# Kernel tuning notes

Measured on AMD Instinct MI355X. Metric: run time of the kernel, lower is better.

The kernel has to match this reference:

```python
import jax, jax.numpy as jnp
import numpy as np

RADIUS = 0.2
NPOINT = 1024
NSAMPLE = 32


def _square_distance(src, dst):
    # src [B,S,C], dst [B,N,C] -> [B,S,N]
    d = -2.0 * jnp.einsum('bsc,bnc->bsn', src, dst)
    d = d + jnp.sum(src * src, -1)[:, :, None]
    d = d + jnp.sum(dst * dst, -1)[:, None, :]
    return d


def _index_points(points, idx):
    # points [B,N,C], idx [B,...] int -> [B,...,C]
    B = points.shape[0]
    flat = idx.reshape(B, -1)
    out = jnp.take_along_axis(points, flat[:, :, None], axis=1)
    return out.reshape(idx.shape + (points.shape[-1],))


def _query_ball_point(radius, nsample, xyz, new_xyz):
    # xyz [B,N,C], new_xyz [B,S,C] -> idx [B,S,nsample]
    B, N, _ = xyz.shape
    sqd = _square_distance(new_xyz, xyz)            # [B,S,N]
    base = jnp.arange(N, dtype=jnp.int32)[None, None, :]
    idx = jnp.where(sqd > radius * radius, N, base)  # out-of-ball -> sentinel N
    idx = jnp.sort(idx, axis=-1)[:, :, :nsample]     # nearest-index nsample in ball
    first = idx[:, :, :1]
    idx = jnp.where(idx == N, first, idx)            # pad with first valid index
    return idx


def setup_inputs() -> dict:
    key = jax.random.key(0)
    ks = jax.random.split(key, 4)
    B, N, D = 8, 8192, 64
    xyz = jax.random.normal(ks[0], (B, 2, N), dtype=jnp.float32)
    points = jax.random.normal(ks[1], (B, D, N), dtype=jnp.float32)
    C_in = D + 2
    W1 = jax.random.normal(ks[2], (128, C_in), dtype=jnp.float32) * (1.0 / np.sqrt(C_in))
    b1 = jnp.zeros((128,), dtype=jnp.float32)
    W2 = jax.random.normal(ks[3], (256, 128), dtype=jnp.float32) * (1.0 / np.sqrt(128))
    b2 = jnp.zeros((256,), dtype=jnp.float32)
    return {"xyz": xyz, "points": points, "W1": W1, "b1": b1, "W2": W2, "b2": b2}


def reference(xyz, points, W1, b1, W2, b2):
    # xyz [B,2,N], points [B,D,N]
    xyz_t = jnp.transpose(xyz, (0, 2, 1))        # [B,N,2]
    pts_t = jnp.transpose(points, (0, 2, 1))     # [B,N,D]
    B, N, C = xyz_t.shape
    S = NPOINT
    # fps_idx = arange(npoint) in the source (deterministic sampling)
    new_xyz = xyz_t[:, :S, :]                    # [B,S,2]
    idx = _query_ball_point(RADIUS, NSAMPLE, xyz_t, new_xyz)   # [B,S,K]
    grouped_xyz = _index_points(xyz_t, idx)                    # [B,S,K,2]
    grouped_xyz_norm = grouped_xyz - new_xyz[:, :, None, :]
    grouped_pts = _index_points(pts_t, idx)                    # [B,S,K,D]
    feat = jnp.concatenate([grouped_xyz_norm, grouped_pts], axis=-1)  # [B,S,K,2+D]
    # permute(0,3,2,1) -> [B, C, K, S]; conv kernel (1,1) == pointwise linear on C
    h = jnp.transpose(feat, (0, 3, 2, 1))                      # [B,C,K,S]
    h = jax.nn.silu(jnp.einsum('bcks,oc->boks', h, W1) + b1[None, :, None, None])
    h = jax.nn.silu(jnp.einsum('bcks,oc->boks', h, W2) + b2[None, :, None, None])
    return h.mean(axis=2)                                      # [B, 256, S]
```

## Files before the change

### kernel.cpp

```cpp
#include <hip/hip_runtime.h>
#include <math.h>

#define BB 8
#define NN 8192
#define SS 1024
#define NS 32
#define DD 64
#define C1 128
#define C2 256
#define R2 0.04f
#define CPB 8

using bf16x8 = __attribute__((ext_vector_type(8))) short;
using f32x4  = __attribute__((ext_vector_type(4))) float;

__device__ __forceinline__ float silu_f(float x) {
    return x / (1.0f + __expf(-x));
}
__device__ __forceinline__ unsigned int f2bf(float f) {
    unsigned int u = __float_as_uint(f);
    u += 0x7fffu + ((u >> 16) & 1u);
    return u >> 16;
}
__device__ __forceinline__ float bfl(unsigned int u) { return __uint_as_float(u << 16); }
__device__ __forceinline__ float bfh(unsigned int u) { return __uint_as_float(u & 0xffff0000u); }

__global__ __launch_bounds__(256) void qbp_kernel(const float* __restrict__ xyz,
                                                  int* __restrict__ idx_ws) {
    int gwave = (blockIdx.x * blockDim.x + threadIdx.x) >> 6;
    int lane  = threadIdx.x & 63;
    int b = gwave >> 10;
    int s = gwave & (SS - 1);
    const float* x = xyz + (size_t)b * 2 * NN;
    const float* y = x + NN;
    float cx = x[s], cy = y[s];
    float cs = __fadd_rn(__fmul_rn(cx, cx), __fmul_rn(cy, cy));
    int* ob = idx_ws + ((size_t)(b * SS + s)) * NS;

    int written = 0;
    int first = -1;
    for (int base = 0; base < NN && written < NS; base += 128) {
        int jA = base + lane, jB = base + 64 + lane;
        float pxA = x[jA], pyA = y[jA];
        float pxB = x[jB], pyB = y[jB];
        float ppA = __fadd_rn(__fmul_rn(pxA, pxA), __fmul_rn(pyA, pyA));
        float eA  = __fadd_rn(__fmul_rn(cx, pxA), __fmul_rn(cy, pyA));
        float dA  = __fadd_rn(__fadd_rn(__fmul_rn(-2.0f, eA), cs), ppA);
        float ppB = __fadd_rn(__fmul_rn(pxB, pxB), __fmul_rn(pyB, pyB));
        float eB  = __fadd_rn(__fmul_rn(cx, pxB), __fmul_rn(cy, pyB));
        float dB  = __fadd_rn(__fadd_rn(__fmul_rn(-2.0f, eB), cs), ppB);
        bool inA = !(dA > R2);
        bool inB = !(dB > R2);
        unsigned long long mA = __ballot(inA);
        unsigned long long mB = __ballot(inB);
        if (first < 0) {
            if (mA)      first = base + (__ffsll(mA) - 1);
            else if (mB) first = base + 64 + (__ffsll(mB) - 1);
        }
        unsigned long long below = (1ull << lane) - 1ull;
        int posA = __popcll(mA & below);
        if (inA && written + posA < NS) ob[written + posA] = jA;
        int wA = written + __popcll(mA);
        int posB = __popcll(mB & below);
        if (inB && wA + posB < NS) ob[wA + posB] = jB;
        written = wA + __popcll(mB);
        if (written > NS) written = NS;
    }
    if (lane >= written && lane < NS) ob[lane] = first;
}

__global__ __launch_bounds__(256) void pack_kernel(const float* __restrict__ W1,
                                                   const float* __restrict__ W2,
                                                   unsigned short* __restrict__ W1p,
                                                   unsigned short* __restrict__ W2p) {
    int bid = blockIdx.x;
    if (bid < 16) {
        int tid = bid * 256 + threadIdx.x;
        int l = tid & 63, frag = tid >> 6;
        int kb = frag >> 4, nt = frag & 15;
        int o  = nt * 16 + (l & 15);
        int c0 = kb * 32 + ((l >> 4) << 3);
        const float* src = W2 + (size_t)o * C1 + c0;
        unsigned int up[4];
        #pragma unroll
        for (int q = 0; q < 4; ++q)
            up[q] = f2bf(src[2 * q]) | (f2bf(src[2 * q + 1]) << 16);
        *(uint4*)(W2p + ((size_t)tid << 3)) = make_uint4(up[0], up[1], up[2], up[3]);
    } else {
        int tid = (bid - 16) * 256 + threadIdx.x;
        int l = tid & 63, frag = tid >> 6;
        int kb = frag >> 3, nt = frag & 7;
        int o  = nt * 16 + (l & 15);
        int c0 = kb * 32 + ((l >> 4) << 3);
        const float* src = W1 + (size_t)o * 66 + 2 + c0;
        unsigned int up[4];
        #pragma unroll
        for (int q = 0; q < 4; ++q)
            up[q] = f2bf(src[2 * q]) | (f2bf(src[2 * q + 1]) << 16);
        *(uint4*)(W1p + ((size_t)tid << 3)) = make_uint4(up[0], up[1], up[2], up[3]);
    }
}

__global__ __launch_bounds__(256) void p1g_kernel(const float* __restrict__ points,
                                                  const unsigned short* __restrict__ W1p,
                                                  const float* __restrict__ b1,
                                                  unsigned short* __restrict__ P1) {
    __shared__ __align__(16) char lds[34816];
    const int t = threadIdx.x;
    const int w = t >> 6, l = t & 63;
    const int bidx = blockIdx.x;
    const int b  = bidx >> 6;
    const int j0 = (bidx & 63) << 7;

    bf16x8 bfr[8][2];
    #pragma unroll
    for (int nt = 0; nt < 8; ++nt)
        #pragma unroll
        for (int kb = 0; kb < 2; ++kb)
            bfr[nt][kb] = *(const bf16x8*)(W1p + (((size_t)((kb * 8 + nt) * 64 + l)) << 3));
    float b1v[8];
    #pragma unroll
    for (int nt = 0; nt < 8; ++nt) b1v[nt] = b1[nt * 16 + (l & 15)];

    {
        const float* pb = points + (size_t)b * DD * NN + j0;
        int jj0 = (t & 31) * 4;
        #pragma unroll
        for (int i = 0; i < 4; ++i) {
            int c = 2 * ((t >> 5) + i * 8);
            float4 q0 = *(const float4*)(pb + (size_t)c * NN + jj0);
            float4 q1 = *(const float4*)(pb + (size_t)(c + 1) * NN + jj0);
            float a0[4] = {q0.x, q0.y, q0.z, q0.w};
            float a1[4] = {q1.x, q1.y, q1.z, q1.w};
            #pragma unroll
            for (int d = 0; d < 4; ++d) {
                int jj = jj0 + d;
                unsigned int u = f2bf(a0[d]) | (f2bf(a1[d]) << 16);
                unsigned int addr = ((unsigned)(jj * 128 + c * 2))
                                    ^ ((unsigned)((((jj & 7) ^ ((jj >> 2) & 7)) << 4)));
                *(unsigned int*)(lds + addr) = u;
            }
        }
    }
    __syncthreads();

    bf16x8 afr[2][2];
    #pragma unroll
    for (int mt = 0; mt < 2; ++mt)
        #pragma unroll
        for (int kb = 0; kb < 2; ++kb) {
            int jg = w * 32 + mt * 16 + (l & 15);
            unsigned int addr = ((unsigned)(jg * 128 + kb * 64 + ((l >> 4) << 4)))
                                ^ ((unsigned)((((jg & 7) ^ ((jg >> 2) & 7)) << 4)));
            afr[mt][kb] = *(const bf16x8*)(lds + addr);
        }
    __syncthreads();

    f32x4 acc[2][8];
    #pragma unroll
    for (int mt = 0; mt < 2; ++mt)
        #pragma unroll
        for (int nt = 0; nt < 8; ++nt) {
            f32x4 z4 = {0.0f, 0.0f, 0.0f, 0.0f};
            acc[mt][nt] = z4;
        }
    #pragma unroll
    for (int kb = 0; kb < 2; ++kb)
        #pragma unroll
        for (int mt = 0; mt < 2; ++mt)
            #pragma unroll
            for (int nt = 0; nt < 8; ++nt)
                acc[mt][nt] = __builtin_amdgcn_mfma_f32_16x16x32_bf16(
                    afr[mt][kb], bfr[nt][kb], acc[mt][nt], 0, 0, 0);

    #pragma unroll
    for (int mt = 0; mt < 2; ++mt)
        #pragma unroll
        for (int nt = 0; nt < 8; ++nt) {
            int row0 = w * 32 + mt * 16 + ((l >> 4) << 2);
            int col  = nt * 16 + (l & 15);
            #pragma unroll
            for (int r = 0; r < 4; ++r) {
                float v = acc[mt][nt][r] + b1v[nt];
                *(unsigned short*)(lds + (size_t)(row0 + r) * 272 + col * 2) =
                    (unsigned short)f2bf(v);
            }
        }
    __syncthreads();

    {
        int row = t >> 1, half = t & 1;
        const char* src = lds + (size_t)row * 272 + half * 128;
        unsigned short* dst = P1 + ((size_t)(b * NN + j0 + row)) * C1 + half * 64;
        #pragma unroll
        for (int i = 0; i < 8; ++i)
            *(uint4*)(dst + i * 8) = *(const uint4*)(src + i * 16);
    }
}

__global__ __launch_bounds__(256) void fused2_kernel(const float* __restrict__ xyz,
                                                     const float* __restrict__ W1,
                                                     const float* __restrict__ b2,
                                                     const unsigned short* __restrict__ P1,
                                                     const int* __restrict__ idx_ws,
                                                     const unsigned short* __restrict__ W2p,
                                                     float* __restrict__ tmp) {
    __shared__ __align__(16) unsigned short H1s[NS * C1];
    __shared__ int   idxs[CPB][NS];
    __shared__ float dxs[CPB][NS], dys[CPB][NS];
    __shared__ float w1xy[2][C1];

    const int t = threadIdx.x;
    const int w = t >> 6, l = t & 63;
    const int gc0 = blockIdx.x * CPB;

    if (t < C1) { w1xy[0][t] = W1[(size_t)t * 66 + 0]; w1xy[1][t] = W1[(size_t)t * 66 + 1]; }
    {
        int ci = t >> 5, kk = t & 31;
        int gc = gc0 + ci;
        int b = gc >> 10, s = gc & (SS - 1);
        const float* x = xyz + (size_t)b * 2 * NN;
        const float* y = x + NN;
        int j = idx_ws[(size_t)gc * NS + kk];
        idxs[ci][kk] = j;
        dxs[ci][kk] = x[j] - x[s];
        dys[ci][kk] = y[j] - y[s];
    }

    bf16x8 bfr[4][4];
    #pragma unroll
    for (int kb = 0; kb < 4; ++kb)
        #pragma unroll
        for (int ntl = 0; ntl < 4; ++ntl) {
            int nt = w * 4 + ntl;
            bfr[ntl][kb] = *(const bf16x8*)(W2p + ((size_t)((kb * 16 + nt) * 64 + l) << 3));
        }
    float b2v[4];
    #pragma unroll
    for (int ntl = 0; ntl < 4; ++ntl) b2v[ntl] = b2[w * 64 + ntl * 16 + (l & 15)];

    __syncthreads();

    const int k = t >> 3, cb = t & 7;
    for (int ci = 0; ci < CPB; ++ci) {
        int gc = gc0 + ci;
        int b = gc >> 10;
        {
            int j = idxs[ci][k];
            float dx = dxs[ci][k], dy = dys[ci][k];
            const uint4* pr = (const uint4*)(P1 + ((size_t)b * NN + j) * C1 + cb * 16);
            uint4 q0 = pr[0], q1 = pr[1];
            float hv[16];
            hv[0]  = bfl(q0.x); hv[1]  = bfh(q0.x);
            hv[2]  = bfl(q0.y); hv[3]  = bfh(q0.y);
            hv[4]  = bfl(q0.z); hv[5]  = bfh(q0.z);
            hv[6]  = bfl(q0.w); hv[7]  = bfh(q0.w);
            hv[8]  = bfl(q1.x); hv[9]  = bfh(q1.x);
            hv[10] = bfl(q1.y); hv[11] = bfh(q1.y);
            hv[12] = bfl(q1.z); hv[13] = bfh(q1.z);
            hv[14] = bfl(q1.w); hv[15] = bfh(q1.w);
            #pragma unroll
            for (int i = 0; i < 16; ++i) {
                int c = cb * 16 + i;
                float v = hv[i] + w1xy[0][c] * dx + w1xy[1][c] * dy;
                hv[i] = silu_f(v);
            }
            unsigned int up[8];
            #pragma unroll
            for (int q = 0; q < 8; ++q)
                up[q] = f2bf(hv[2 * q]) | (f2bf(hv[2 * q + 1]) << 16);
            unsigned int swz = (unsigned)((k & 7) << 4);
            unsigned int a0 = ((unsigned)(k * 256 + cb * 32)) ^ swz;
            unsigned int a1 = ((unsigned)(k * 256 + cb * 32 + 16)) ^ swz;
            *(uint4*)((char*)H1s + a0) = make_uint4(up[0], up[1], up[2], up[3]);
            *(uint4*)((char*)H1s + a1) = make_uint4(up[4], up[5], up[6], up[7]);
        }
        __syncthreads();
        bf16x8 afr[2][4];
        #pragma unroll
        for (int mt = 0; mt < 2; ++mt)
            #pragma unroll
            for (int kb = 0; kb < 4; ++kb) {
                int m = mt * 16 + (l & 15);
                unsigned int addr = ((unsigned)(m * 256 + kb * 64 + ((l >> 4) << 4)))
                                    ^ ((unsigned)((m & 7) << 4));
                afr[mt][kb] = *(const bf16x8*)((char*)H1s + addr);
            }
        f32x4 acc[2][4];
        #pragma unroll
        for (int mt = 0; mt < 2; ++mt)
            #pragma unroll
            for (int ntl = 0; ntl < 4; ++ntl) {
                f32x4 z4 = {0.0f, 0.0f, 0.0f, 0.0f};
                acc[mt][ntl] = z4;
            }
        #pragma unroll
        for (int kb = 0; kb < 4; ++kb)
            #pragma unroll
            for (int mt = 0; mt < 2; ++mt)
                #pragma unroll
                for (int ntl = 0; ntl < 4; ++ntl)
                    acc[mt][ntl] = __builtin_amdgcn_mfma_f32_16x16x32_bf16(
                        afr[mt][kb], bfr[ntl][kb], acc[mt][ntl], 0, 0, 0);
        float po[4];
        #pragma unroll
        for (int ntl = 0; ntl < 4; ++ntl) {
            float sum = 0.0f;
            #pragma unroll
            for (int mt = 0; mt < 2; ++mt)
                #pragma unroll
                for (int r = 0; r < 4; ++r)
                    sum += silu_f(acc[mt][ntl][r] + b2v[ntl]);
            sum += __shfl_xor(sum, 16);
            sum += __shfl_xor(sum, 32);
            po[ntl] = sum * (1.0f / 32.0f);
        }
        if (l < 16) {
            #pragma unroll
            for (int ntl = 0; ntl < 4; ++ntl)
                tmp[(size_t)gc * C2 + w * 64 + ntl * 16 + l] = po[ntl];
        }
        __syncthreads();
    }
}

__global__ __launch_bounds__(256) void transpose_kernel(const float* __restrict__ tmp,
                                                        float* __restrict__ out) {
    __shared__ float tile[32][33];
    int bid = blockIdx.x;
    int b  = bid >> 8;
    int r  = bid & 255;
    int s0 = (r >> 3) << 5;
    int o0 = (r & 7) << 5;
    int t = threadIdx.x;
    int c = t & 31, rr = t >> 5;
    const float* tb = tmp + (size_t)b * SS * C2;
    #pragma unroll
    for (int i = 0; i < 4; ++i) {
        int row = rr + i * 8;
        tile[row][c] = tb[(size_t)(s0 + row) * C2 + o0 + c];
    }
    __syncthreads();
    float* ob = out + (size_t)b * C2 * SS;
    #pragma unroll
    for (int i = 0; i < 4; ++i) {
        int row = rr + i * 8;
        ob[(size_t)(o0 + row) * SS + s0 + c] = tile[c][row];
    }
}

extern "C" void kernel_launch(void* const* d_in, const int* in_sizes, int n_in,
                              void* d_out, int out_size, void* d_ws, size_t ws_size,
                              hipStream_t stream) {
    const float* xyz    = (const float*)d_in[0];
    const float* points = (const float*)d_in[1];
    const float* W1     = (const float*)d_in[2];
    const float* b1     = (const float*)d_in[3];
    const float* W2     = (const float*)d_in[4];
    const float* b2     = (const float*)d_in[5];
    float* out = (float*)d_out;

    const size_t OFF_W1P = 65536;
    const size_t OFF_IDX = OFF_W1P + 16384;
    const size_t OFF_P1  = OFF_IDX + (size_t)BB * SS * NS * sizeof(int);
    const size_t OFF_TMP = OFF_P1 + (size_t)BB * NN * C1 * sizeof(unsigned short);

    unsigned short* W2p = (unsigned short*)d_ws;
    unsigned short* W1p = (unsigned short*)((char*)d_ws + OFF_W1P);
    int*            idx = (int*)((char*)d_ws + OFF_IDX);
    unsigned short* P1  = (unsigned short*)((char*)d_ws + OFF_P1);
    float*          tmp = (float*)((char*)d_ws + OFF_TMP);

    qbp_kernel   <<<BB * SS / 4,     256, 0, stream>>>(xyz, idx);
    pack_kernel  <<<20,              256, 0, stream>>>(W1, W2, W1p, W2p);
    p1g_kernel   <<<BB * (NN / 128), 256, 0, stream>>>(points, W1p, b1, P1);
    fused2_kernel<<<BB * SS / CPB,   256, 0, stream>>>(xyz, W1, b2, P1, idx, W2p, tmp);
    transpose_kernel<<<BB * (SS / 32) * (C2 / 32), 256, 0, stream>>>(tmp, out);
}
```

Baseline: 187.7 us.

## Double-buffer H1 tiles, prefetch qbp loads, fast SiLU, halve centroids per block

The fused MLP kernel now double-buffers the H1 shared tile. The next centroid's gather and layer-1 SiLU overlap the current centroid's MFMA and reduction, with one barrier per iteration instead of two. The ball-query kernel software-prefetches the next chunk of coordinates. SiLU uses raw v_exp/v_rcp instructions, and centroids per block drop from 8 to 4, giving more blocks. The trade-offs are more LDS and registers per block and slightly less accurate exp and reciprocal.

```diff
diff --git a/kernel.cpp b/kernel.cpp
--- a/kernel.cpp
+++ b/kernel.cpp
@@ -9,13 +9,19 @@
 #define C1 128
 #define C2 256
 #define R2 0.04f
-#define CPB 8
+#define CPB 4
 
 using bf16x8 = __attribute__((ext_vector_type(8))) short;
 using f32x4  = __attribute__((ext_vector_type(4))) float;
 
+__device__ __forceinline__ float rcp_f(float v) {
+    float r; asm("v_rcp_f32 %0, %1" : "=v"(r) : "v"(v)); return r;
+}
+__device__ __forceinline__ float exp2_f(float v) {
+    float r; asm("v_exp_f32 %0, %1" : "=v"(r) : "v"(v)); return r;
+}
 __device__ __forceinline__ float silu_f(float x) {
-    return x / (1.0f + __expf(-x));
+    return x * rcp_f(1.0f + exp2_f(x * -1.44269504088896f));
 }
 __device__ __forceinline__ unsigned int f2bf(float f) {
     unsigned int u = __float_as_uint(f);
@@ -37,12 +43,17 @@
     float cs = __fadd_rn(__fmul_rn(cx, cx), __fmul_rn(cy, cy));
     int* ob = idx_ws + ((size_t)(b * SS + s)) * NS;
 
+    float pxA = x[lane],      pyA = y[lane];
+    float pxB = x[64 + lane], pyB = y[64 + lane];
+
     int written = 0;
     int first = -1;
     for (int base = 0; base < NN && written < NS; base += 128) {
-        int jA = base + lane, jB = base + 64 + lane;
-        float pxA = x[jA], pyA = y[jA];
-        float pxB = x[jB], pyB = y[jB];
+        int jA2 = base + 128 + lane;      if (jA2 >= NN) jA2 = NN - 1;
+        int jB2 = base + 192 + lane;      if (jB2 >= NN) jB2 = NN - 1;
+        float nxA = x[jA2], nyA = y[jA2];
+        float nxB = x[jB2], nyB = y[jB2];
+
         float ppA = __fadd_rn(__fmul_rn(pxA, pxA), __fmul_rn(pyA, pyA));
         float eA  = __fadd_rn(__fmul_rn(cx, pxA), __fmul_rn(cy, pyA));
         float dA  = __fadd_rn(__fadd_rn(__fmul_rn(-2.0f, eA), cs), ppA);
@@ -59,12 +70,14 @@
         }
         unsigned long long below = (1ull << lane) - 1ull;
         int posA = __popcll(mA & below);
-        if (inA && written + posA < NS) ob[written + posA] = jA;
+        if (inA && written + posA < NS) ob[written + posA] = base + lane;
         int wA = written + __popcll(mA);
         int posB = __popcll(mB & below);
-        if (inB && wA + posB < NS) ob[wA + posB] = jB;
+        if (inB && wA + posB < NS) ob[wA + posB] = base + 64 + lane;
         written = wA + __popcll(mB);
         if (written > NS) written = NS;
+
+        pxA = nxA; pyA = nyA; pxB = nxB; pyB = nyB;
     }
     if (lane >= written && lane < NS) ob[lane] = first;
 }
@@ -205,20 +218,24 @@
                                                      const int* __restrict__ idx_ws,
                                                      const unsigned short* __restrict__ W2p,
                                                      float* __restrict__ tmp) {
-    __shared__ __align__(16) unsigned short H1s[NS * C1];
+    __shared__ __align__(16) unsigned short H1s[2][NS * C1];
     __shared__ int   idxs[CPB][NS];
     __shared__ float dxs[CPB][NS], dys[CPB][NS];
-    __shared__ float w1xy[2][C1];
+    __shared__ float w1xy[C1][2];
 
     const int t = threadIdx.x;
     const int w = t >> 6, l = t & 63;
     const int gc0 = blockIdx.x * CPB;
-
-    if (t < C1) { w1xy[0][t] = W1[(size_t)t * 66 + 0]; w1xy[1][t] = W1[(size_t)t * 66 + 1]; }
-    {
+    const int b   = gc0 >> 10;
+
+    if (t < C1) {
+        w1xy[t][0] = W1[(size_t)t * 66 + 0];
+        w1xy[t][1] = W1[(size_t)t * 66 + 1];
+    }
+    if (t < CPB * NS) {
         int ci = t >> 5, kk = t & 31;
         int gc = gc0 + ci;
-        int b = gc >> 10, s = gc & (SS - 1);
+        int s = gc & (SS - 1);
         const float* x = xyz + (size_t)b * 2 * NN;
         const float* y = x + NN;
         int j = idx_ws[(size_t)gc * NS + kk];
@@ -242,14 +259,83 @@
     __syncthreads();
 
     const int k = t >> 3, cb = t & 7;
-    for (int ci = 0; ci < CPB; ++ci) {
-        int gc = gc0 + ci;
-        int b = gc >> 10;
-        {
-            int j = idxs[ci][k];
-            float dx = dxs[ci][k], dy = dys[ci][k];
-            const uint4* pr = (const uint4*)(P1 + ((size_t)b * NN + j) * C1 + cb * 16);
-            uint4 q0 = pr[0], q1 = pr[1];
+    float wx[16], wy[16];
+    #pragma unroll
+    for (int i = 0; i < 16; ++i) {
+        wx[i] = w1xy[cb * 16 + i][0];
+        wy[i] = w1xy[cb * 16 + i][1];
+    }
+    const unsigned int swz = (unsigned)((k & 7) << 4);
+    const unsigned int sa0 = ((unsigned)(k * 256 + cb * 32)) ^ swz;
+    const unsigned int sa1 = ((unsigned)(k * 256 + cb * 32 + 16)) ^ swz;
+    unsigned int afr_addr[2][4];
+    #pragma unroll
+    for (int mt = 0; mt < 2; ++mt)
+        #pragma unroll
+        for (int kb = 0; kb < 4; ++kb) {
+            int m = mt * 16 + (l & 15);
+            afr_addr[mt][kb] = ((unsigned)(m * 256 + kb * 64 + ((l >> 4) << 4)))
+                               ^ ((unsigned)((m & 7) << 4));
+        }
+    const unsigned short* P1b = P1 + (size_t)b * NN * C1 + cb * 16;
+
+    for (int ci = -1; ci < CPB; ++ci) {
+        const bool have = (ci + 1 < CPB);
+
+        uint4 q0, q1; float dx = 0.0f, dy = 0.0f;
+        if (have) {
+            int j = idxs[ci + 1][k];
+            dx = dxs[ci + 1][k]; dy = dys[ci + 1][k];
+            const uint4* pr = (const uint4*)(P1b + (size_t)j * C1);
+            q0 = pr[0]; q1 = pr[1];
+        }
+
+        if (ci >= 0) {
+            const char* bufr = (const char*)H1s[ci & 1];
+            bf16x8 afr[2][4];
+            #pragma unroll
+            for (int mt = 0; mt < 2; ++mt)
+                #pragma unroll
+                for (int kb = 0; kb < 4; ++kb)
+                    afr[mt][kb] = *(const bf16x8*)(bufr + afr_addr[mt][kb]);
+            f32x4 acc[2][4];
+            #pragma unroll
+            for (int mt = 0; mt < 2; ++mt)
+                #pragma unroll
+                for (int ntl = 0; ntl < 4; ++ntl) {
+                    f32x4 z4 = {0.0f, 0.0f, 0.0f, 0.0f};
+                    acc[mt][ntl] = z4;
+                }
+            #pragma unroll
+            for (int kb = 0; kb < 4; ++kb)
+                #pragma unroll
+                for (int mt = 0; mt < 2; ++mt)
+                    #pragma unroll
+                    for (int ntl = 0; ntl < 4; ++ntl)
+                        acc[mt][ntl] = __builtin_amdgcn_mfma_f32_16x16x32_bf16(
+                            afr[mt][kb], bfr[ntl][kb], acc[mt][ntl], 0, 0, 0);
+            float po[4];
+            #pragma unroll
+            for (int ntl = 0; ntl < 4; ++ntl) {
+                float sum = 0.0f;
+                #pragma unroll
+                for (int mt = 0; mt < 2; ++mt)
+                    #pragma unroll
+                    for (int r = 0; r < 4; ++r)
+                        sum += silu_f(acc[mt][ntl][r] + b2v[ntl]);
+                sum += __shfl_xor(sum, 16);
+                sum += __shfl_xor(sum, 32);
+                po[ntl] = sum * (1.0f / 32.0f);
+            }
+            if (l < 16) {
+                int gc = gc0 + ci;
+                #pragma unroll
+                for (int ntl = 0; ntl < 4; ++ntl)
+                    tmp[(size_t)gc * C2 + w * 64 + ntl * 16 + l] = po[ntl];
+            }
+        }
+
+        if (have) {
             float hv[16];
             hv[0]  = bfl(q0.x); hv[1]  = bfh(q0.x);
             hv[2]  = bfl(q0.y); hv[3]  = bfh(q0.y);
@@ -261,64 +347,16 @@
             hv[14] = bfl(q1.w); hv[15] = bfh(q1.w);
             #pragma unroll
             for (int i = 0; i < 16; ++i) {
-                int c = cb * 16 + i;
-                float v = hv[i] + w1xy[0][c] * dx + w1xy[1][c] * dy;
+                float v = hv[i] + wx[i] * dx + wy[i] * dy;
                 hv[i] = silu_f(v);
             }
             unsigned int up[8];
             #pragma unroll
             for (int q = 0; q < 8; ++q)
                 up[q] = f2bf(hv[2 * q]) | (f2bf(hv[2 * q + 1]) << 16);
-            unsigned int swz = (unsigned)((k & 7) << 4);
-            unsigned int a0 = ((unsigned)(k * 256 + cb * 32)) ^ swz;
-            unsigned int a1 = ((unsigned)(k * 256 + cb * 32 + 16)) ^ swz;
-            *(uint4*)((char*)H1s + a0) = make_uint4(up[0], up[1], up[2], up[3]);
-            *(uint4*)((char*)H1s + a1) = make_uint4(up[4], up[5], up[6], up[7]);
-        }
-        __syncthreads();
-        bf16x8 afr[2][4];
-        #pragma unroll
-        for (int mt = 0; mt < 2; ++mt)
-            #pragma unroll
-            for (int kb = 0; kb < 4; ++kb) {
-                int m = mt * 16 + (l & 15);
-                unsigned int addr = ((unsigned)(m * 256 + kb * 64 + ((l >> 4) << 4)))
-                                    ^ ((unsigned)((m & 7) << 4));
-                afr[mt][kb] = *(const bf16x8*)((char*)H1s + addr);
-            }
-        f32x4 acc[2][4];
-        #pragma unroll
-        for (int mt = 0; mt < 2; ++mt)
-            #pragma unroll
-            for (int ntl = 0; ntl < 4; ++ntl) {
-                f32x4 z4 = {0.0f, 0.0f, 0.0f, 0.0f};
-                acc[mt][ntl] = z4;
-            }
-        #pragma unroll
-        for (int kb = 0; kb < 4; ++kb)
-            #pragma unroll
-            for (int mt = 0; mt < 2; ++mt)
-                #pragma unroll
-                for (int ntl = 0; ntl < 4; ++ntl)
-                    acc[mt][ntl] = __builtin_amdgcn_mfma_f32_16x16x32_bf16(
-                        afr[mt][kb], bfr[ntl][kb], acc[mt][ntl], 0, 0, 0);
-        float po[4];
-        #pragma unroll
-        for (int ntl = 0; ntl < 4; ++ntl) {
-            float sum = 0.0f;
-            #pragma unroll
-            for (int mt = 0; mt < 2; ++mt)
-                #pragma unroll
-                for (int r = 0; r < 4; ++r)
-                    sum += silu_f(acc[mt][ntl][r] + b2v[ntl]);
-            sum += __shfl_xor(sum, 16);
-            sum += __shfl_xor(sum, 32);
-            po[ntl] = sum * (1.0f / 32.0f);
-        }
-        if (l < 16) {
-            #pragma unroll
-            for (int ntl = 0; ntl < 4; ++ntl)
-                tmp[(size_t)gc * C2 + w * 64 + ntl * 16 + l] = po[ntl];
+            char* bufw = (char*)H1s[(ci + 1) & 1];
+            *(uint4*)(bufw + sa0) = make_uint4(up[0], up[1], up[2], up[3]);
+            *(uint4*)(bufw + sa1) = make_uint4(up[4], up[5], up[6], up[7]);
         }
         __syncthreads();
     }
```

After: 162.6 us. 1.15x faster.
